# Optimization experiments

Measured on AMD Instinct MI355X. Metric: run time of the kernel, lower is better.

## Reference

```python
import jax, jax.numpy as jnp
import numpy as np

RADIUS = 0.05
HMIN = -0.02
HMAXES = (0.01, 0.02, 0.03, 0.04)
NSAMPLE = 64
BN_EPS = 1e-5


def _group(d_rot, hmax):
    # d_rot: (B,S,N,3) seed-relative coords rotated into the gripper frame (d @ R)
    # Cylinder query: approach axis is x; keep first NSAMPLE points with
    # y^2+z^2 < r^2 and hmin < x < hmax; pad with first hit (0 if no hit),
    # matching the CUDA cylinder_query kernel semantics.
    N = d_rot.shape[2]
    h = d_rot[..., 0]
    r2 = d_rot[..., 1] ** 2 + d_rot[..., 2] ** 2
    mask = (r2 < RADIUS * RADIUS) & (h > HMIN) & (h < hmax)
    key = jnp.where(mask, jnp.arange(N, dtype=jnp.int32), N)
    neg_top, _ = jax.lax.top_k(-key, NSAMPLE)   # ascending keys = first hits in point order
    idx = -neg_top                               # (B,S,k); == N where slot is invalid
    first = idx[..., :1]
    idx = jnp.where(idx < N, idx, jnp.where(first < N, first, 0))
    return jnp.take_along_axis(d_rot, idx[..., None], axis=2)  # (B,S,k,3)


def _mlp_layer(x, w, b, g, be, m, v):
    # 1x1 Conv2d + BatchNorm (eval-mode, running stats) + ReLU, as in pt_utils.SharedMLP
    x = jnp.einsum('bcpn,oc->bopn', x, w) + b[None, :, None, None]
    scale = g / jnp.sqrt(v + BN_EPS)
    x = (x - m[None, :, None, None]) * scale[None, :, None, None] + be[None, :, None, None]
    return jax.nn.relu(x)


def _forward(seed_xyz, pointcloud, vp_rot, params):
    B, S, _ = seed_xyz.shape
    D = len(HMAXES)
    d = pointcloud[:, None, :, :] - seed_xyz[:, :, None, :]          # (B,S,N,3)
    d_rot = jnp.einsum('bsnc,bscd->bsnd', d, vp_rot)                 # rotate into gripper frame
    groups = jnp.stack([_group(d_rot, h) for h in HMAXES], axis=2)   # (B,S,D,k,3)
    x = groups.transpose(0, 4, 1, 2, 3).reshape(B, 3, S * D, NSAMPLE)  # (B,3,S*D,k)
    for (w, b, g, be, m, v) in params:
        x = _mlp_layer(x, w, b, g, be, m, v)
    x = x.max(axis=-1)                                               # max-pool over nsample
    return x.reshape(B, -1, S, D)                                    # (B,256,S,D)


def setup_inputs() -> dict:
    key = jax.random.key(0)
    ks = jax.random.split(key, 8)
    B, S, N = 2, 1024, 16384
    inp = {
        'seed_xyz': jax.random.uniform(ks[0], (B, S, 3), jnp.float32),
        'pointcloud': jax.random.uniform(ks[1], (B, N, 3), jnp.float32),
        'vp_rot': jax.random.normal(ks[2], (B, S, 3, 3), jnp.float32),
    }
    dims = [3, 64, 128, 256]
    for i in range(3):
        cin, cout = dims[i], dims[i + 1]
        k1, k2, k3, k4, k5, k6 = jax.random.split(ks[3 + i], 6)
        inp[f'w{i+1}'] = jax.random.normal(k1, (cout, cin), jnp.float32) * 0.05
        inp[f'b{i+1}'] = jax.random.normal(k2, (cout,), jnp.float32) * 0.01
        inp[f'g{i+1}'] = 1.0 + 0.1 * jax.random.normal(k3, (cout,), jnp.float32)
        inp[f'be{i+1}'] = jax.random.normal(k4, (cout,), jnp.float32) * 0.01
        inp[f'm{i+1}'] = jax.random.normal(k5, (cout,), jnp.float32) * 0.01
        inp[f'v{i+1}'] = jax.random.uniform(k6, (cout,), jnp.float32, 0.5, 1.5)
    return inp


def reference(seed_xyz, pointcloud, vp_rot,
              w1, b1, g1, be1, m1, v1,
              w2, b2, g2, be2, m2, v2,
              w3, b3, g3, be3, m3, v3):
    params = [(w1, b1, g1, be1, m1, v1),
              (w2, b2, g2, be2, m2, v2),
              (w3, b3, g3, be3, m3, v3)]
    return _forward(seed_xyz, pointcloud, vp_rot, params)
```

## Files before the change

### kernel.cpp

```cpp
#include <hip/hip_runtime.h>
#include <hip/hip_bf16.h>
#include <cstdint>
#include <cstddef>

#define NSAMP  64
#define NPT    16384
#define NLVL   4
#define NCHUNK 8
#define CHSZ   (NPT / NCHUNK)

typedef __attribute__((ext_vector_type(8))) short  short8;
typedef __attribute__((ext_vector_type(4))) float  floatx4;
typedef __attribute__((ext_vector_type(4))) unsigned int uintx4;
typedef __attribute__((ext_vector_type(2))) unsigned int uintx2;

__device__ __forceinline__ unsigned short f2bf(float x) {
    union { float f; unsigned int u; } c; c.f = x;
    unsigned int r = (c.u + 0x7fffu + ((c.u >> 16) & 1u)) >> 16;
    return (unsigned short)r;
}
__device__ __forceinline__ unsigned int f2bf2(float a, float b) {
    __hip_bfloat162 t = __float22bfloat162_rn(make_float2(a, b));
    union { __hip_bfloat162 h; unsigned int u; } c; c.h = t;
    return c.u;
}

__global__ __launch_bounds__(256) void prep_kernel(
    const float* __restrict__ w1, const float* __restrict__ b1, const float* __restrict__ g1,
    const float* __restrict__ be1, const float* __restrict__ m1, const float* __restrict__ v1,
    const float* __restrict__ w2, const float* __restrict__ b2, const float* __restrict__ g2,
    const float* __restrict__ be2, const float* __restrict__ m2, const float* __restrict__ v2,
    const float* __restrict__ w3, const float* __restrict__ b3, const float* __restrict__ g3,
    const float* __restrict__ be3, const float* __restrict__ m3, const float* __restrict__ v3,
    float* __restrict__ w1f, float* __restrict__ fb1,
    unsigned short* __restrict__ w2b, float* __restrict__ fb2,
    unsigned short* __restrict__ w3b, float* __restrict__ fb3)
{
    const int t  = blockIdx.x * 256 + threadIdx.x;
    const int nt = gridDim.x * 256;
    const float eps = 1e-5f;
    for (int i = t; i < 64 * 3; i += nt)    w1f[i] = w1[i] * (g1[i / 3] / sqrtf(v1[i / 3] + eps));
    for (int i = t; i < 64; i += nt)        fb1[i] = (b1[i] - m1[i]) * (g1[i] / sqrtf(v1[i] + eps)) + be1[i];
    for (int i = t; i < 128 * 64; i += nt)  w2b[i] = f2bf(w2[i] * (g2[i / 64] / sqrtf(v2[i / 64] + eps)));
    for (int i = t; i < 128; i += nt)       fb2[i] = (b2[i] - m2[i]) * (g2[i] / sqrtf(v2[i] + eps)) + be2[i];
    for (int i = t; i < 256 * 128; i += nt) w3b[i] = f2bf(w3[i] * (g3[i / 128] / sqrtf(v3[i / 128] + eps)));
    for (int i = t; i < 256; i += nt)       fb3[i] = (b3[i] - m3[i]) * (g3[i] / sqrtf(v3[i] + eps)) + be3[i];
}

__global__ __launch_bounds__(512) void scan_kernel(
    const float* __restrict__ seedp, const float* __restrict__ pc,
    const float* __restrict__ rot, unsigned short* __restrict__ buf,
    int* __restrict__ cnts)
{
    __shared__ float ch[CHSZ * 3];
    const int tid  = threadIdx.x;
    const int lane = tid & 63;
    const int w    = tid >> 6;
    const int sg   = blockIdx.x >> 3;
    const int c    = blockIdx.x & 7;
    const int g    = sg * 8 + w;
    const int b    = g >> 10;

    {
        const float4* src = (const float4*)(pc + ((size_t)b * NPT + c * CHSZ) * 3);
        float4* dst = (float4*)ch;
        dst[tid]        = src[tid];
        dst[tid + 512]  = src[tid + 512];
        dst[tid + 1024] = src[tid + 1024];
    }
    __syncthreads();

    const float* sd = seedp + (size_t)g * 3;
    const float sx = sd[0], sy = sd[1], sz = sd[2];
    const float* R = rot + (size_t)g * 9;
    const float r00 = R[0], r01 = R[1], r02 = R[2];
    const float r10 = R[3], r11 = R[4], r12 = R[5];
    const float r20 = R[6], r21 = R[7], r22 = R[8];
    const float nc0 = -(sx * r00 + sy * r10 + sz * r20);
    const float nc1 = -(sx * r01 + sy * r11 + sz * r21);
    const float nc2 = -(sx * r02 + sy * r12 + sz * r22);

    unsigned short* bufg = buf + (size_t)g * (NLVL * NCHUNK * 64);
    int cnt0 = 0, cnt1 = 0, cnt2 = 0, cnt3 = 0;
    const unsigned long long lm = (1ull << lane) - 1ull;

    for (int bt = 0; bt < 4; ++bt) {
        float pxv[8], pyv[8], pzv[8];
        #pragma unroll
        for (int j = 0; j < 8; ++j) {
            const int pl = (bt * 8 + j) * 64 + lane;
            pxv[j] = ch[pl * 3];
            pyv[j] = ch[pl * 3 + 1];
            pzv[j] = ch[pl * 3 + 2];
        }
        #pragma unroll
        for (int j = 0; j < 8; ++j) {
            const float h = fmaf(pxv[j], r00, fmaf(pyv[j], r10, fmaf(pzv[j], r20, nc0)));
            const float u = fmaf(pxv[j], r01, fmaf(pyv[j], r11, fmaf(pzv[j], r21, nc1)));
            const float v = fmaf(pxv[j], r02, fmaf(pyv[j], r12, fmaf(pzv[j], r22, nc2)));
            const float r2 = fmaf(u, u, v * v);
            const bool base = (r2 < 0.0025f) && (h > -0.02f) && (h < 0.04f);

            const unsigned long long bal3 = __ballot(base);
            if (bal3 == 0ull) continue;

            const unsigned short pidx = (unsigned short)(c * CHSZ + (bt * 8 + j) * 64 + lane);
            #pragma unroll
            for (int l = 0; l < NLVL; ++l) {
                unsigned long long bal; bool m;
                if (l == 3) { m = base; bal = bal3; }
                else {
                    const float hm = (l == 0) ? 0.01f : (l == 1) ? 0.02f : 0.03f;
                    m = base && (h < hm);
                    bal = __ballot(m);
                }
                int& cnt = (l == 0) ? cnt0 : (l == 1) ? cnt1 : (l == 2) ? cnt2 : cnt3;
                if (m) {
                    const int pos = cnt + (int)__popcll(bal & lm);
                    if (pos < 64) bufg[(l * NCHUNK + c) * 64 + pos] = pidx;
                }
                cnt += (int)__popcll(bal);
            }
        }
        if (cnt0 >= NSAMP) break;
    }

    if (lane == 0) {
        int* cg = cnts + (size_t)g * (NLVL * NCHUNK);
        cg[0 * NCHUNK + c] = cnt0;
        cg[1 * NCHUNK + c] = cnt1;
        cg[2 * NCHUNK + c] = cnt2;
        cg[3 * NCHUNK + c] = cnt3;
    }
}

__global__ __launch_bounds__(256) void gather_kernel(
    const float* __restrict__ seedp, const float* __restrict__ pc,
    const float* __restrict__ rot,
    const unsigned short* __restrict__ buf, const int* __restrict__ cnts,
    float* __restrict__ gx)
{
    const int n = threadIdx.x & 63;
    const int W = blockIdx.x * 4 + (threadIdx.x >> 6);
    const int g = W >> 2, l = W & 3;
    const int b = g >> 10;

    const int* cg = cnts + (size_t)g * (NLVL * NCHUNK) + l * NCHUNK;
    const unsigned short* bl = buf + (size_t)g * (NLVL * NCHUNK * 64) + l * (NCHUNK * 64);
    int idx = -1, acc = 0, firstIdx = -1;
    #pragma unroll
    for (int c = 0; c < NCHUNK; ++c) {
        const int cn = min(cg[c], 64);
        if (cn > 0 && firstIdx < 0) firstIdx = (int)bl[c * 64];
        if (n >= acc && n < acc + cn) idx = (int)bl[c * 64 + (n - acc)];
        acc += cn;
    }
    if (idx < 0) idx = (firstIdx >= 0) ? firstIdx : 0;

    const float* sd = seedp + (size_t)g * 3;
    const float* R  = rot   + (size_t)g * 9;
    const float* pp = pc + ((size_t)b * NPT + idx) * 3;
    const float dx = pp[0] - sd[0], dy = pp[1] - sd[1], dz = pp[2] - sd[2];

    float* o = gx + (size_t)W * 192;
    o[n]       = dx * R[0] + dy * R[3] + dz * R[6];
    o[64 + n]  = dx * R[1] + dy * R[4] + dz * R[7];
    o[128 + n] = dx * R[2] + dy * R[5] + dz * R[8];
}

__global__ __launch_bounds__(256) void mlp_kernel(
    const float* __restrict__ gx,
    const float* __restrict__ w1f, const float* __restrict__ fb1,
    const unsigned short* __restrict__ w2b, const float* __restrict__ fb2,
    const unsigned short* __restrict__ w3b, const float* __restrict__ fb3,
    float* __restrict__ out)
{
    __shared__ unsigned short lds[8192];
    unsigned short* h1t = lds;
    unsigned short* h2t = lds;

    const int tid = threadIdx.x;
    const int n      = tid & 63;
    const int w      = tid >> 6;
    const int lane15 = tid & 15;
    const int quad   = (tid & 63) >> 4;

    short8 wa3[4][4];
    float  wb3[4];
    #pragma unroll
    for (int mt = 0; mt < 4; ++mt) {
        const int m0 = (w * 4 + mt) * 16;
        #pragma unroll
        for (int k0 = 0; k0 < 4; ++k0)
            wa3[mt][k0] = *(const short8*)&w3b[(m0 + lane15) * 128 + k0 * 32 + quad * 8];
        wb3[mt] = fb3[m0 + lane15];
    }

    for (int it = 0; it < 4; ++it) {
        const int gp = blockIdx.x * 4 + it;
        const int g = gp >> 2, l = gp & 3;
        const int b = g >> 10, s = g & 1023;

        short8 a20[2], a21[2]; floatx4 b2v[2];
        #pragma unroll
        for (int mi = 0; mi < 2; ++mi) {
            const int m0 = (w * 2 + mi) * 16;
            a20[mi] = *(const short8*)&w2b[(m0 + lane15) * 64 + quad * 8];
            a21[mi] = *(const short8*)&w2b[(m0 + lane15) * 64 + 32 + quad * 8];
            b2v[mi] = *(const floatx4*)&fb2[m0 + quad * 4];
        }

        {
            const float* xb = gx + (size_t)gp * 192;
            const float x0 = xb[n], x1 = xb[64 + n], x2 = xb[128 + n];
            unsigned int p[8];
            #pragma unroll
            for (int j = 0; j < 8; ++j) {
                const int o0 = __builtin_amdgcn_readfirstlane(w * 16 + 2 * j);
                const float a0 = fb1[o0]     + w1f[o0*3]*x0   + w1f[o0*3+1]*x1 + w1f[o0*3+2]*x2;
                const float a1 = fb1[o0 + 1] + w1f[o0*3+3]*x0 + w1f[o0*3+4]*x1 + w1f[o0*3+5]*x2;
                p[j] = f2bf2(fmaxf(a0, 0.f), fmaxf(a1, 0.f));
            }
            *(uintx4*)&h1t[(((w * 2)    ) * 64 + n) * 8] = (uintx4){p[0], p[1], p[2], p[3]};
            *(uintx4*)&h1t[(((w * 2) + 1) * 64 + n) * 8] = (uintx4){p[4], p[5], p[6], p[7]};
        }
        __syncthreads();

        {
            short8 bfr[4][2];
            #pragma unroll
            for (int nt = 0; nt < 4; ++nt)
                #pragma unroll
                for (int k0 = 0; k0 < 2; ++k0)
                    bfr[nt][k0] = *(const short8*)&h1t[((k0 * 4 + quad) * 64 + nt * 16 + lane15) * 8];
            __syncthreads();

            #pragma unroll
            for (int mi = 0; mi < 2; ++mi) {
                const int m0 = (w * 2 + mi) * 16;
                #pragma unroll
                for (int nt = 0; nt < 4; ++nt) {
                    floatx4 acc = b2v[mi];
                    acc = __builtin_amdgcn_mfma_f32_16x16x32_bf16(a20[mi], bfr[nt][0], acc, 0, 0, 0);
                    acc = __builtin_amdgcn_mfma_f32_16x16x32_bf16(a21[mi], bfr[nt][1], acc, 0, 0, 0);
                    const int n2 = nt * 16 + lane15;
                    const unsigned int q0 = f2bf2(fmaxf(acc[0], 0.f), fmaxf(acc[1], 0.f));
                    const unsigned int q1 = f2bf2(fmaxf(acc[2], 0.f), fmaxf(acc[3], 0.f));
                    const int kb = (m0 >> 3) + (quad >> 1);
                    *(uintx2*)&h2t[(kb * 64 + n2) * 8 + (quad & 1) * 4] = (uintx2){q0, q1};
                }
            }
        }
        __syncthreads();

        {
            short8 bfr[4][4];
            #pragma unroll
            for (int nt = 0; nt < 4; ++nt)
                #pragma unroll
                for (int k0 = 0; k0 < 4; ++k0)
                    bfr[nt][k0] = *(const short8*)&h2t[((k0 * 4 + quad) * 64 + nt * 16 + lane15) * 8];

            #pragma unroll
            for (int mt = 0; mt < 4; ++mt) {
                const int m0 = (w * 4 + mt) * 16;
                floatx4 acc[4];
                #pragma unroll
                for (int nt = 0; nt < 4; ++nt) acc[nt] = (floatx4){0.f, 0.f, 0.f, 0.f};
                #pragma unroll
                for (int k0 = 0; k0 < 4; ++k0)
                    #pragma unroll
                    for (int nt = 0; nt < 4; ++nt)
                        acc[nt] = __builtin_amdgcn_mfma_f32_16x16x32_bf16(bfr[nt][k0], wa3[mt][k0], acc[nt], 0, 0, 0);

                float t0 = fmaxf(fmaxf(acc[0][0], acc[0][1]), fmaxf(acc[0][2], acc[0][3]));
                float t1 = fmaxf(fmaxf(acc[1][0], acc[1][1]), fmaxf(acc[1][2], acc[1][3]));
                float t2 = fmaxf(fmaxf(acc[2][0], acc[2][1]), fmaxf(acc[2][2], acc[2][3]));
                float t3 = fmaxf(fmaxf(acc[3][0], acc[3][1]), fmaxf(acc[3][2], acc[3][3]));
                float t  = fmaxf(fmaxf(t0, t1), fmaxf(t2, t3));
                t = fmaxf(t, __shfl_xor(t, 16));
                t = fmaxf(t, __shfl_xor(t, 32));
                if (quad == 0) {
                    const int o = m0 + lane15;
                    out[(((size_t)b * 256 + o) * 1024 + s) * 4 + l] = fmaxf(t + wb3[mt], 0.f);
                }
            }
        }
        __syncthreads();
    }
}

extern "C" void kernel_launch(void* const* d_in, const int* in_sizes, int n_in,
                              void* d_out, int out_size, void* d_ws, size_t ws_size,
                              hipStream_t stream) {
    const float* seed = (const float*)d_in[0];
    const float* pc   = (const float*)d_in[1];
    const float* rot  = (const float*)d_in[2];
    const float* w1 = (const float*)d_in[3];
    const float* b1 = (const float*)d_in[4];
    const float* g1 = (const float*)d_in[5];
    const float* be1 = (const float*)d_in[6];
    const float* m1 = (const float*)d_in[7];
    const float* v1 = (const float*)d_in[8];
    const float* w2 = (const float*)d_in[9];
    const float* b2 = (const float*)d_in[10];
    const float* g2 = (const float*)d_in[11];
    const float* be2 = (const float*)d_in[12];
    const float* m2 = (const float*)d_in[13];
    const float* v2 = (const float*)d_in[14];
    const float* w3 = (const float*)d_in[15];
    const float* b3 = (const float*)d_in[16];
    const float* g3 = (const float*)d_in[17];
    const float* be3 = (const float*)d_in[18];
    const float* m3 = (const float*)d_in[19];
    const float* v3 = (const float*)d_in[20];

    float* w1f = (float*)d_ws;
    float* fb1 = w1f + 192;
    float* fb2 = fb1 + 64;
    float* fb3 = fb2 + 128;
    unsigned short* w2b = (unsigned short*)(fb3 + 256);
    unsigned short* w3b = w2b + 8192;
    unsigned short* buf = w3b + 32768;
    int* cnts = (int*)(buf + 4194304);
    float* gx = (float*)(cnts + 65536);

    prep_kernel<<<64, 256, 0, stream>>>(w1, b1, g1, be1, m1, v1,
                                        w2, b2, g2, be2, m2, v2,
                                        w3, b3, g3, be3, m3, v3,
                                        w1f, fb1, w2b, fb2, w3b, fb3);
    scan_kernel<<<2048, 512, 0, stream>>>(seed, pc, rot, buf, cnts);
    gather_kernel<<<2048, 256, 0, stream>>>(seed, pc, rot, buf, cnts, gx);
    mlp_kernel<<<2048, 256, 0, stream>>>(gx, w1f, fb1, w2b, fb2, w3b, fb3,
                                         (float*)d_out);
}
```

Before: 188.3 us.

## Fuse cylinder scan and gather into one kernel with per-seed blocks

```diff
diff --git a/kernel.cpp b/kernel.cpp
--- a/kernel.cpp
+++ b/kernel.cpp
@@ -47,28 +47,18 @@
     for (int i = t; i < 256; i += nt)       fb3[i] = (b3[i] - m3[i]) * (g3[i] / sqrtf(v3[i] + eps)) + be3[i];
 }
 
-__global__ __launch_bounds__(512) void scan_kernel(
+__global__ __launch_bounds__(512) void scangather_kernel(
     const float* __restrict__ seedp, const float* __restrict__ pc,
-    const float* __restrict__ rot, unsigned short* __restrict__ buf,
-    int* __restrict__ cnts)
+    const float* __restrict__ rot, float* __restrict__ gx)
 {
-    __shared__ float ch[CHSZ * 3];
+    __shared__ unsigned short slist[NCHUNK][NLVL][64];
+    __shared__ int scnt[NCHUNK][NLVL];
+
     const int tid  = threadIdx.x;
     const int lane = tid & 63;
-    const int w    = tid >> 6;
-    const int sg   = blockIdx.x >> 3;
-    const int c    = blockIdx.x & 7;
-    const int g    = sg * 8 + w;
+    const int c    = tid >> 6;
+    const int g    = blockIdx.x;
     const int b    = g >> 10;
-
-    {
-        const float4* src = (const float4*)(pc + ((size_t)b * NPT + c * CHSZ) * 3);
-        float4* dst = (float4*)ch;
-        dst[tid]        = src[tid];
-        dst[tid + 512]  = src[tid + 512];
-        dst[tid + 1024] = src[tid + 1024];
-    }
-    __syncthreads();
 
     const float* sd = seedp + (size_t)g * 3;
     const float sx = sd[0], sy = sd[1], sz = sd[2];
@@ -80,92 +70,83 @@
     const float nc1 = -(sx * r01 + sy * r11 + sz * r21);
     const float nc2 = -(sx * r02 + sy * r12 + sz * r22);
 
-    unsigned short* bufg = buf + (size_t)g * (NLVL * NCHUNK * 64);
+    const float* pcb = pc + (size_t)b * NPT * 3;
+    const unsigned long long lm = (1ull << lane) - 1ull;
     int cnt0 = 0, cnt1 = 0, cnt2 = 0, cnt3 = 0;
-    const unsigned long long lm = (1ull << lane) - 1ull;
-
-    for (int bt = 0; bt < 4; ++bt) {
-        float pxv[8], pyv[8], pzv[8];
+    const int base = c * CHSZ;
+
+    for (int it = 0; it < CHSZ / 256; ++it) {
+        const int p0 = base + it * 256 + lane * 4;
+        const float4 q0 = *(const float4*)(pcb + (size_t)p0 * 3);
+        const float4 q1 = *(const float4*)(pcb + (size_t)p0 * 3 + 4);
+        const float4 q2 = *(const float4*)(pcb + (size_t)p0 * 3 + 8);
+
+        float hh[4]; bool bm[4];
+        {
+            const float px[4] = {q0.x, q0.w, q1.z, q2.y};
+            const float py[4] = {q0.y, q1.x, q1.w, q2.z};
+            const float pz[4] = {q0.z, q1.y, q2.x, q2.w};
+            #pragma unroll
+            for (int j = 0; j < 4; ++j) {
+                const float h = fmaf(px[j], r00, fmaf(py[j], r10, fmaf(pz[j], r20, nc0)));
+                const float u = fmaf(px[j], r01, fmaf(py[j], r11, fmaf(pz[j], r21, nc1)));
+                const float v = fmaf(px[j], r02, fmaf(py[j], r12, fmaf(pz[j], r22, nc2)));
+                const float r2 = fmaf(u, u, v * v);
+                hh[j] = h;
+                bm[j] = (r2 < 0.0025f) && (h > -0.02f) && (h < 0.04f);
+            }
+        }
+        if (__ballot(bm[0] || bm[1] || bm[2] || bm[3]) == 0ull) continue;
+
         #pragma unroll
-        for (int j = 0; j < 8; ++j) {
-            const int pl = (bt * 8 + j) * 64 + lane;
-            pxv[j] = ch[pl * 3];
-            pyv[j] = ch[pl * 3 + 1];
-            pzv[j] = ch[pl * 3 + 2];
-        }
+        for (int l = 0; l < NLVL; ++l) {
+            const float hm = (l == 0) ? 0.01f : (l == 1) ? 0.02f : (l == 2) ? 0.03f : 0.04f;
+            const bool m0 = bm[0] && (hh[0] < hm);
+            const bool m1 = bm[1] && (hh[1] < hm);
+            const bool m2 = bm[2] && (hh[2] < hm);
+            const bool m3 = bm[3] && (hh[3] < hm);
+            const unsigned long long b0 = __ballot(m0);
+            const unsigned long long b1 = __ballot(m1);
+            const unsigned long long b2 = __ballot(m2);
+            const unsigned long long b3 = __ballot(m3);
+            int& cnt = (l == 0) ? cnt0 : (l == 1) ? cnt1 : (l == 2) ? cnt2 : cnt3;
+            const int lanePref = (int)(__popcll(b0 & lm) + __popcll(b1 & lm) +
+                                       __popcll(b2 & lm) + __popcll(b3 & lm));
+            int own = 0;
+            if (m0) { const int pos = cnt + lanePref;       if (pos < 64) slist[c][l][pos] = (unsigned short)(p0);     own = 1; }
+            if (m1) { const int pos = cnt + lanePref + own; if (pos < 64) slist[c][l][pos] = (unsigned short)(p0 + 1); ++own; }
+            if (m2) { const int pos = cnt + lanePref + own; if (pos < 64) slist[c][l][pos] = (unsigned short)(p0 + 2); ++own; }
+            if (m3) { const int pos = cnt + lanePref + own; if (pos < 64) slist[c][l][pos] = (unsigned short)(p0 + 3); ++own; }
+            cnt += (int)(__popcll(b0) + __popcll(b1) + __popcll(b2) + __popcll(b3));
+        }
+        if (cnt0 >= NSAMP) break;
+    }
+    if (lane < NLVL) {
+        const int cnt = (lane == 0) ? cnt0 : (lane == 1) ? cnt1 : (lane == 2) ? cnt2 : cnt3;
+        scnt[c][lane] = cnt;
+    }
+    __syncthreads();
+
+    if (c < NLVL) {
+        const int l = c;
+        const int n = lane;
+        int idx = -1, acc = 0, firstIdx = -1;
         #pragma unroll
-        for (int j = 0; j < 8; ++j) {
-            const float h = fmaf(pxv[j], r00, fmaf(pyv[j], r10, fmaf(pzv[j], r20, nc0)));
-            const float u = fmaf(pxv[j], r01, fmaf(pyv[j], r11, fmaf(pzv[j], r21, nc1)));
-            const float v = fmaf(pxv[j], r02, fmaf(pyv[j], r12, fmaf(pzv[j], r22, nc2)));
-            const float r2 = fmaf(u, u, v * v);
-            const bool base = (r2 < 0.0025f) && (h > -0.02f) && (h < 0.04f);
-
-            const unsigned long long bal3 = __ballot(base);
-            if (bal3 == 0ull) continue;
-
-            const unsigned short pidx = (unsigned short)(c * CHSZ + (bt * 8 + j) * 64 + lane);
-            #pragma unroll
-            for (int l = 0; l < NLVL; ++l) {
-                unsigned long long bal; bool m;
-                if (l == 3) { m = base; bal = bal3; }
-                else {
-                    const float hm = (l == 0) ? 0.01f : (l == 1) ? 0.02f : 0.03f;
-                    m = base && (h < hm);
-                    bal = __ballot(m);
-                }
-                int& cnt = (l == 0) ? cnt0 : (l == 1) ? cnt1 : (l == 2) ? cnt2 : cnt3;
-                if (m) {
-                    const int pos = cnt + (int)__popcll(bal & lm);
-                    if (pos < 64) bufg[(l * NCHUNK + c) * 64 + pos] = pidx;
-                }
-                cnt += (int)__popcll(bal);
-            }
-        }
-        if (cnt0 >= NSAMP) break;
-    }
-
-    if (lane == 0) {
-        int* cg = cnts + (size_t)g * (NLVL * NCHUNK);
-        cg[0 * NCHUNK + c] = cnt0;
-        cg[1 * NCHUNK + c] = cnt1;
-        cg[2 * NCHUNK + c] = cnt2;
-        cg[3 * NCHUNK + c] = cnt3;
-    }
-}
-
-__global__ __launch_bounds__(256) void gather_kernel(
-    const float* __restrict__ seedp, const float* __restrict__ pc,
-    const float* __restrict__ rot,
-    const unsigned short* __restrict__ buf, const int* __restrict__ cnts,
-    float* __restrict__ gx)
-{
-    const int n = threadIdx.x & 63;
-    const int W = blockIdx.x * 4 + (threadIdx.x >> 6);
-    const int g = W >> 2, l = W & 3;
-    const int b = g >> 10;
-
-    const int* cg = cnts + (size_t)g * (NLVL * NCHUNK) + l * NCHUNK;
-    const unsigned short* bl = buf + (size_t)g * (NLVL * NCHUNK * 64) + l * (NCHUNK * 64);
-    int idx = -1, acc = 0, firstIdx = -1;
-    #pragma unroll
-    for (int c = 0; c < NCHUNK; ++c) {
-        const int cn = min(cg[c], 64);
-        if (cn > 0 && firstIdx < 0) firstIdx = (int)bl[c * 64];
-        if (n >= acc && n < acc + cn) idx = (int)bl[c * 64 + (n - acc)];
-        acc += cn;
-    }
-    if (idx < 0) idx = (firstIdx >= 0) ? firstIdx : 0;
-
-    const float* sd = seedp + (size_t)g * 3;
-    const float* R  = rot   + (size_t)g * 9;
-    const float* pp = pc + ((size_t)b * NPT + idx) * 3;
-    const float dx = pp[0] - sd[0], dy = pp[1] - sd[1], dz = pp[2] - sd[2];
-
-    float* o = gx + (size_t)W * 192;
-    o[n]       = dx * R[0] + dy * R[3] + dz * R[6];
-    o[64 + n]  = dx * R[1] + dy * R[4] + dz * R[7];
-    o[128 + n] = dx * R[2] + dy * R[5] + dz * R[8];
+        for (int ck = 0; ck < NCHUNK; ++ck) {
+            const int cn = min(scnt[ck][l], 64);
+            if (cn > 0 && firstIdx < 0) firstIdx = (int)slist[ck][l][0];
+            if (n >= acc && n < acc + cn) idx = (int)slist[ck][l][n - acc];
+            acc += cn;
+        }
+        if (idx < 0) idx = (firstIdx >= 0) ? firstIdx : 0;
+
+        const float* pp = pcb + (size_t)idx * 3;
+        const float dx = pp[0] - sx, dy = pp[1] - sy, dz = pp[2] - sz;
+        float* o = gx + ((size_t)g * 4 + l) * 192;
+        o[n]       = dx * r00 + dy * r10 + dz * r20;
+        o[64 + n]  = dx * r01 + dy * r11 + dz * r21;
+        o[128 + n] = dx * r02 + dy * r12 + dz * r22;
+    }
 }
 
 __global__ __launch_bounds__(256) void mlp_kernel(
@@ -321,16 +302,13 @@
     float* fb3 = fb2 + 128;
     unsigned short* w2b = (unsigned short*)(fb3 + 256);
     unsigned short* w3b = w2b + 8192;
-    unsigned short* buf = w3b + 32768;
-    int* cnts = (int*)(buf + 4194304);
-    float* gx = (float*)(cnts + 65536);
+    float* gx = (float*)(w3b + 32768);
 
     prep_kernel<<<64, 256, 0, stream>>>(w1, b1, g1, be1, m1, v1,
                                         w2, b2, g2, be2, m2, v2,
                                         w3, b3, g3, be3, m3, v3,
                                         w1f, fb1, w2b, fb2, w3b, fb3);
-    scan_kernel<<<2048, 512, 0, stream>>>(seed, pc, rot, buf, cnts);
-    gather_kernel<<<2048, 256, 0, stream>>>(seed, pc, rot, buf, cnts, gx);
+    scangather_kernel<<<2048, 512, 0, stream>>>(seed, pc, rot, gx);
     mlp_kernel<<<2048, 256, 0, stream>>>(gx, w1f, fb1, w2b, fb2, w3b, fb3,
                                          (float*)d_out);
 }
```

New measurement: 192.4 us. 1.02x slower.
